# Performance work log

Measured on AMD Instinct MI355X. Metric: run time of the kernel, lower is better.

## Reference

```python
import jax, jax.numpy as jnp
import numpy as np

N_NODES = 50000
N_EDGES = 800000
IN_DIM = 128
HID = 64
HEADS = 4
OUT = 16
N_GRAPHS = 500
NEG_SLOPE = 0.2


def setup_inputs() -> dict:
    key = jax.random.key(0)
    ks = jax.random.split(key, 12)
    x = jax.random.normal(ks[0], (N_NODES, IN_DIM), dtype=jnp.float32)
    edge_index = jax.random.randint(ks[1], (2, N_EDGES), 0, N_NODES, dtype=jnp.int64)
    batch = jnp.sort(jax.random.randint(ks[2], (N_NODES,), 0, N_GRAPHS, dtype=jnp.int64))
    s1 = 1.0 / np.sqrt(IN_DIM)
    s2 = 1.0 / np.sqrt(HID)
    W1 = jax.random.normal(ks[3], (IN_DIM, HEADS * HID), dtype=jnp.float32) * s1
    a1_src = jax.random.normal(ks[4], (HEADS, HID), dtype=jnp.float32) * s2
    a1_dst = jax.random.normal(ks[5], (HEADS, HID), dtype=jnp.float32) * s2
    b1 = jnp.zeros((HID,), dtype=jnp.float32)
    W2 = jax.random.normal(ks[6], (HID, HEADS * HID), dtype=jnp.float32) * s2
    a2_src = jax.random.normal(ks[7], (HEADS, HID), dtype=jnp.float32) * s2
    a2_dst = jax.random.normal(ks[8], (HEADS, HID), dtype=jnp.float32) * s2
    b2 = jnp.zeros((HID,), dtype=jnp.float32)
    fcW = jax.random.normal(ks[9], (HID, OUT), dtype=jnp.float32) * s2
    fcb = jnp.zeros((OUT,), dtype=jnp.float32)
    return {"x": x, "edge_index": edge_index, "batch": batch,
            "W1": W1, "a1_src": a1_src, "a1_dst": a1_dst, "b1": b1,
            "W2": W2, "a2_src": a2_src, "a2_dst": a2_dst, "b2": b2,
            "fcW": fcW, "fcb": fcb}


def gat_conv(x, W, a_src, a_dst, b, src, dst):
    # PyG GATConv with concat=False: per-head linear, edge softmax over dst, head-mean.
    n = x.shape[0]
    h = (x @ W).reshape(n, HEADS, HID)          # [N,H,D]
    alpha_s = jnp.sum(h * a_src, axis=-1)        # [N,H]
    alpha_d = jnp.sum(h * a_dst, axis=-1)        # [N,H]
    e = jax.nn.leaky_relu(alpha_s[src] + alpha_d[dst], NEG_SLOPE)  # [E,H]
    emax = jax.ops.segment_max(e, dst, num_segments=n)
    ex = jnp.exp(e - emax[dst])
    denom = jax.ops.segment_sum(ex, dst, num_segments=n)
    alpha = ex / denom[dst]                      # [E,H], edge softmax per dst
    msg = h[src] * alpha[:, :, None]             # [E,H,D]
    out = jax.ops.segment_sum(msg, dst, num_segments=n)  # [N,H,D]
    return out.mean(axis=1) + b                  # concat=False -> head mean


def reference(x, edge_index, batch, W1, a1_src, a1_dst, b1, W2, a2_src, a2_dst, b2, fcW, fcb):
    n = x.shape[0]
    # PyG GATConv default add_self_loops=True
    loops = jnp.arange(n, dtype=edge_index.dtype)
    src = jnp.concatenate([edge_index[0], loops])
    dst = jnp.concatenate([edge_index[1], loops])
    h = jax.nn.relu(gat_conv(x, W1, a1_src, a1_dst, b1, src, dst))
    h = jax.nn.relu(gat_conv(h, W2, a2_src, a2_dst, b2, src, dst))
    # global_mean_pool over batch ids
    sums = jax.ops.segment_sum(h, batch, num_segments=N_GRAPHS)
    counts = jax.ops.segment_sum(jnp.ones((n,), dtype=h.dtype), batch, num_segments=N_GRAPHS)
    pooled = sums / jnp.clip(counts, 1.0)[:, None]
    return pooled @ fcW + fcb
```

## Files before the change

### kernel.cpp

```cpp
#include <hip/hip_runtime.h>
#include <hip/hip_bf16.h>
#include <hip/hip_fp16.h>

#define NN 50000
#define EE 800000
#define ETOT 850000
#define NG 500
#define NBLK ((NN + 255) / 256)

typedef __attribute__((ext_vector_type(8))) short bf16x8;
typedef __attribute__((ext_vector_type(4))) float f32x4;

__device__ __forceinline__ unsigned short bf16_rne(float v) {
    unsigned u = __float_as_uint(v);
    unsigned r = u + 0x7FFFu + ((u >> 16) & 1u);
    return (unsigned short)(r >> 16);
}

__device__ __forceinline__ int detect_stride(const int* __restrict__ ei,
                                             int tid, int* sflag) {
    if (tid < 64) {
        unsigned long long b = __ballot(ei[2 * tid + 1] != 0);
        if (tid == 0) *sflag = b ? 1 : 2;
    }
    __syncthreads();
    return *sflag;
}

__global__ __launch_bounds__(256) void k_prep(const int* __restrict__ ei,
                                              int* __restrict__ src32,
                                              int* __restrict__ dst32,
                                              int* __restrict__ deg) {
    __shared__ int sflag;
    int tid = threadIdx.x;
    int st = detect_stride(ei, tid, &sflag);
    int e = blockIdx.x * 256 + tid;
    if (e >= ETOT) return;
    int s, d;
    if (e < EE) {
        s = ei[(size_t)st * e];
        d = ei[(size_t)st * (EE + e)];
    } else {
        s = d = e - EE;
    }
    src32[e] = s;
    dst32[e] = d;
    atomicAdd(&deg[d], 1);
}

__global__ __launch_bounds__(256) void k_blocksum(const int* __restrict__ deg,
                                                  int* __restrict__ bsum) {
    __shared__ int l[256];
    int gid = blockIdx.x * 256 + threadIdx.x;
    int tid = threadIdx.x;
    l[tid] = (gid < NN) ? deg[gid] : 0;
    __syncthreads();
    for (int o = 128; o > 0; o >>= 1) {
        if (tid < o) l[tid] += l[tid + o];
        __syncthreads();
    }
    if (tid == 0) bsum[blockIdx.x] = l[0];
}

__global__ __launch_bounds__(256) void k_scan_bsum(const int* __restrict__ bsum,
                                                   int* __restrict__ boff) {
    __shared__ int l[256];
    int tid = threadIdx.x;
    int v = (tid < NBLK) ? bsum[tid] : 0;
    l[tid] = v;
    __syncthreads();
    for (int d = 1; d < 256; d <<= 1) {
        int t = (tid >= d) ? l[tid - d] : 0;
        __syncthreads();
        l[tid] += t;
        __syncthreads();
    }
    if (tid < NBLK) boff[tid] = l[tid] - v;
}

__global__ __launch_bounds__(256) void k_scan_final(const int* __restrict__ deg,
                                                    const int* __restrict__ boff,
                                                    int* __restrict__ rowptr,
                                                    int* __restrict__ cursor) {
    __shared__ int l[256];
    int gid = blockIdx.x * 256 + threadIdx.x;
    int tid = threadIdx.x;
    int v = (gid < NN) ? deg[gid] : 0;
    l[tid] = v;
    __syncthreads();
    for (int d = 1; d < 256; d <<= 1) {
        int t = (tid >= d) ? l[tid - d] : 0;
        __syncthreads();
        l[tid] += t;
        __syncthreads();
    }
    int ex = l[tid] - v + boff[blockIdx.x];
    if (gid < NN) { rowptr[gid] = ex; cursor[gid] = ex; }
    if (gid == 0) rowptr[NN] = ETOT;
}

__global__ __launch_bounds__(256) void k_scatter(const int* __restrict__ src32,
                                                 const int* __restrict__ dst32,
                                                 int* __restrict__ cursor,
                                                 int* __restrict__ csr_src) {
    int e = blockIdx.x * 256 + threadIdx.x;
    if (e >= ETOT) return;
    int pos = atomicAdd(&cursor[dst32[e]], 1);
    csr_src[pos] = src32[e];
}

__device__ __forceinline__ void prepw_one(const float* __restrict__ W,
                                          const float* __restrict__ asrc,
                                          const float* __restrict__ adst,
                                          unsigned short* __restrict__ bhi,
                                          unsigned short* __restrict__ blo,
                                          float* __restrict__ ap,
                                          float* __restrict__ adp,
                                          int K, int t) {
    int j = t / K, k = t - j * K;
    int d = j >> 2, h = j & 3;
    float v = W[k * 256 + h * 64 + d];
    unsigned short hb = bf16_rne(v);
    float hf = __uint_as_float((unsigned)hb << 16);
    bhi[t] = hb;
    blo[t] = bf16_rne(v - hf);
    if (k == 0) { ap[j] = asrc[h * 64 + d]; adp[j] = adst[h * 64 + d]; }
}

__global__ __launch_bounds__(256) void k_prepw(
        const float* __restrict__ W1, const float* __restrict__ a1s,
        const float* __restrict__ a1d, const float* __restrict__ W2,
        const float* __restrict__ a2s, const float* __restrict__ a2d,
        unsigned short* __restrict__ b1h, unsigned short* __restrict__ b1l,
        unsigned short* __restrict__ b2h, unsigned short* __restrict__ b2l,
        float* __restrict__ ap1, float* __restrict__ adp1,
        float* __restrict__ ap2, float* __restrict__ adp2) {
    int g = blockIdx.x;
    if (g < 128) {
        prepw_one(W1, a1s, a1d, b1h, b1l, ap1, adp1, 128, g * 256 + threadIdx.x);
    } else {
        prepw_one(W2, a2s, a2d, b2h, b2l, ap2, adp2, 64, (g - 128) * 256 + threadIdx.x);
    }
}

template <int K>
__global__ __launch_bounds__(64) void k_gemm_mfma(
        const float* __restrict__ A,
        const unsigned short* __restrict__ Bhi,
        const unsigned short* __restrict__ Blo,
        const float* __restrict__ aperm,
        const float* __restrict__ adperm,
        __half* __restrict__ C16,
        float* __restrict__ os,
        float* __restrict__ od, int M) {
    const int NC = K / 32;
    int lane = threadIdx.x;
    int l = lane & 15, q = lane >> 4;
    int m0 = blockIdx.x * 32;

    bf16x8 ahi[2][NC], alo[2][NC];
#pragma unroll
    for (int t = 0; t < 2; ++t) {
        int row = m0 + t * 16 + l;
        if (row >= M) row = M - 1;
        const float* arow = A + (size_t)row * K + q * 8;
#pragma unroll
        for (int c = 0; c < NC; ++c) {
            float4 v0 = *(const float4*)(arow + c * 32);
            float4 v1 = *(const float4*)(arow + c * 32 + 4);
            float vv[8] = {v0.x, v0.y, v0.z, v0.w, v1.x, v1.y, v1.z, v1.w};
#pragma unroll
            for (int j = 0; j < 8; ++j) {
                unsigned short hb = bf16_rne(vv[j]);
                float hf = __uint_as_float((unsigned)hb << 16);
                ahi[t][c][j] = (short)hb;
                alo[t][c][j] = (short)bf16_rne(vv[j] - hf);
            }
        }
    }

    float ps[2][4] = {}, pd[2][4] = {};
    const size_t brow = (size_t)l * K + q * 8;
#pragma unroll 2
    for (int n = 0; n < 16; ++n) {
        const unsigned short* bh = Bhi + (size_t)(n * 16) * K + brow;
        const unsigned short* bl = Blo + (size_t)(n * 16) * K + brow;
        bf16x8 bhf[NC], blf[NC];
#pragma unroll
        for (int c = 0; c < NC; ++c) {
            bhf[c] = *(const bf16x8*)(bh + c * 32);
            blf[c] = *(const bf16x8*)(bl + c * 32);
        }
        f32x4 acc0 = {0.f, 0.f, 0.f, 0.f}, acc1 = {0.f, 0.f, 0.f, 0.f};
#pragma unroll
        for (int c = 0; c < NC; ++c) {
            acc0 = __builtin_amdgcn_mfma_f32_16x16x32_bf16(ahi[0][c], bhf[c], acc0, 0, 0, 0);
            acc1 = __builtin_amdgcn_mfma_f32_16x16x32_bf16(ahi[1][c], bhf[c], acc1, 0, 0, 0);
            acc0 = __builtin_amdgcn_mfma_f32_16x16x32_bf16(ahi[0][c], blf[c], acc0, 0, 0, 0);
            acc1 = __builtin_amdgcn_mfma_f32_16x16x32_bf16(ahi[1][c], blf[c], acc1, 0, 0, 0);
            acc0 = __builtin_amdgcn_mfma_f32_16x16x32_bf16(alo[0][c], bhf[c], acc0, 0, 0, 0);
            acc1 = __builtin_amdgcn_mfma_f32_16x16x32_bf16(alo[1][c], bhf[c], acc1, 0, 0, 0);
        }
        float av = aperm[n * 16 + l], dv = adperm[n * 16 + l];
#pragma unroll
        for (int r = 0; r < 4; ++r) {
            ps[0][r] += acc0[r] * av; pd[0][r] += acc0[r] * dv;
            ps[1][r] += acc1[r] * av; pd[1][r] += acc1[r] * dv;
            int gm0 = m0 + q * 4 + r;
            if (gm0 < M) C16[(size_t)gm0 * 256 + n * 16 + l] = __float2half(acc0[r]);
            int gm1 = m0 + 16 + q * 4 + r;
            if (gm1 < M) C16[(size_t)gm1 * 256 + n * 16 + l] = __float2half(acc1[r]);
        }
    }
#pragma unroll
    for (int t = 0; t < 2; ++t)
#pragma unroll
        for (int r = 0; r < 4; ++r) {
            ps[t][r] += __shfl_xor(ps[t][r], 4);
            ps[t][r] += __shfl_xor(ps[t][r], 8);
            pd[t][r] += __shfl_xor(pd[t][r], 4);
            pd[t][r] += __shfl_xor(pd[t][r], 8);
        }
    if (l < 4) {
#pragma unroll
        for (int t = 0; t < 2; ++t)
#pragma unroll
            for (int r = 0; r < 4; ++r) {
                int gm = m0 + t * 16 + q * 4 + r;
                if (gm < M) {
                    os[(size_t)gm * 4 + l] = ps[t][r];
                    od[(size_t)gm * 4 + l] = pd[t][r];
                }
            }
    }
}

__device__ __forceinline__ float lrelu_exp(float x) {
    x = x > 0.f ? x : 0.2f * x;
    return __expf(x);
}

__global__ __launch_bounds__(256) void k_aggr(const int* __restrict__ rowptr,
                                              const int* __restrict__ csr_src,
                                              const float* __restrict__ as_,
                                              const float* __restrict__ ad_,
                                              const __half* __restrict__ h16,
                                              const float* __restrict__ bias,
                                              float* __restrict__ out) {
    __shared__ float als[4][256];
    __shared__ int sss[4][64];
    int w = threadIdx.x >> 6;
    int lane = threadIdx.x & 63;
    int d = blockIdx.x * 4 + w;
    if (d >= NN) return;
    int beg = rowptr[d], end = rowptr[d + 1];
    float4 adv = *(const float4*)(ad_ + d * 4);

    int s0 = 0;
    float4 u0 = make_float4(0.f, 0.f, 0.f, 0.f);
    float4 den = make_float4(0.f, 0.f, 0.f, 0.f);
    int i0 = beg + lane;
    if (i0 < end) {
        s0 = csr_src[i0];
        float4 sv = *(const float4*)(as_ + s0 * 4);
        u0.x = lrelu_exp(sv.x + adv.x);
        u0.y = lrelu_exp(sv.y + adv.y);
        u0.z = lrelu_exp(sv.z + adv.z);
        u0.w = lrelu_exp(sv.w + adv.w);
        den = u0;
    }
    for (int i = i0 + 64; i < end; i += 64) {
        int s = csr_src[i];
        float4 sv = *(const float4*)(as_ + s * 4);
        den.x += lrelu_exp(sv.x + adv.x);
        den.y += lrelu_exp(sv.y + adv.y);
        den.z += lrelu_exp(sv.z + adv.z);
        den.w += lrelu_exp(sv.w + adv.w);
    }
#pragma unroll
    for (int off = 32; off > 0; off >>= 1) {
        den.x += __shfl_xor(den.x, off);
        den.y += __shfl_xor(den.y, off);
        den.z += __shfl_xor(den.z, off);
        den.w += __shfl_xor(den.w, off);
    }
    float4 dinv = make_float4(0.25f / den.x, 0.25f / den.y,
                              0.25f / den.z, 0.25f / den.w);
    float4 al0 = make_float4(u0.x * dinv.x, u0.y * dinv.y,
                             u0.z * dinv.z, u0.w * dinv.w);
    *(float4*)&als[w][lane * 4] = al0;
    sss[w][lane] = s0;

    int cnt = end - beg;
    if (cnt > 64) cnt = 64;
    int cnt4 = (cnt + 3) & ~3;
    float acc = 0.f;
    int4 sq = *(const int4*)&sss[w][0];
    uint2 r0 = *(const uint2*)(h16 + (size_t)sq.x * 256 + lane * 4);
    uint2 r1 = *(const uint2*)(h16 + (size_t)sq.y * 256 + lane * 4);
    uint2 r2 = *(const uint2*)(h16 + (size_t)sq.z * 256 + lane * 4);
    uint2 r3 = *(const uint2*)(h16 + (size_t)sq.w * 256 + lane * 4);
    for (int j = 0; j < cnt4; j += 4) {
        int jn = (j + 4) & 63;
        int4 sn = *(const int4*)&sss[w][jn];
        uint2 n0 = *(const uint2*)(h16 + (size_t)sn.x * 256 + lane * 4);
        uint2 n1 = *(const uint2*)(h16 + (size_t)sn.y * 256 + lane * 4);
        uint2 n2 = *(const uint2*)(h16 + (size_t)sn.z * 256 + lane * 4);
        uint2 n3 = *(const uint2*)(h16 + (size_t)sn.w * 256 + lane * 4);
        float4 a0 = *(const float4*)&als[w][j * 4];
        float4 a1 = *(const float4*)&als[w][j * 4 + 4];
        float4 a2 = *(const float4*)&als[w][j * 4 + 8];
        float4 a3 = *(const float4*)&als[w][j * 4 + 12];
        float2 fa, fb;
        fa = __half22float2(*(const __half2*)&r0.x);
        fb = __half22float2(*(const __half2*)&r0.y);
        acc += a0.x * fa.x + a0.y * fa.y + a0.z * fb.x + a0.w * fb.y;
        fa = __half22float2(*(const __half2*)&r1.x);
        fb = __half22float2(*(const __half2*)&r1.y);
        acc += a1.x * fa.x + a1.y * fa.y + a1.z * fb.x + a1.w * fb.y;
        fa = __half22float2(*(const __half2*)&r2.x);
        fb = __half22float2(*(const __half2*)&r2.y);
        acc += a2.x * fa.x + a2.y * fa.y + a2.z * fb.x + a2.w * fb.y;
        fa = __half22float2(*(const __half2*)&r3.x);
        fb = __half22float2(*(const __half2*)&r3.y);
        acc += a3.x * fa.x + a3.y * fa.y + a3.z * fb.x + a3.w * fb.y;
        r0 = n0; r1 = n1; r2 = n2; r3 = n3;
    }
    for (int chunk = beg + 64; chunk < end; chunk += 64) {
        int i = chunk + lane;
        int s = 0;
        float4 al = make_float4(0.f, 0.f, 0.f, 0.f);
        if (i < end) {
            s = csr_src[i];
            float4 sv = *(const float4*)(as_ + s * 4);
            al.x = lrelu_exp(sv.x + adv.x) * dinv.x;
            al.y = lrelu_exp(sv.y + adv.y) * dinv.y;
            al.z = lrelu_exp(sv.z + adv.z) * dinv.z;
            al.w = lrelu_exp(sv.w + adv.w) * dinv.w;
        }
        int cc = end - chunk;
        if (cc > 64) cc = 64;
        for (int j = 0; j < cc; ++j) {
            int sj = __shfl(s, j);
            float a0 = __shfl(al.x, j), a1 = __shfl(al.y, j);
            float a2 = __shfl(al.z, j), a3 = __shfl(al.w, j);
            uint2 raw = *(const uint2*)(h16 + (size_t)sj * 256 + lane * 4);
            float2 fa = __half22float2(*(const __half2*)&raw.x);
            float2 fb = __half22float2(*(const __half2*)&raw.y);
            acc += a0 * fa.x + a1 * fa.y + a2 * fb.x + a3 * fb.y;
        }
    }
    float v = acc + bias[lane];
    out[d * 64 + lane] = v > 0.f ? v : 0.f;
}

__global__ __launch_bounds__(256) void k_pool_fc(const float* __restrict__ x3,
                                                 const int* __restrict__ batch,
                                                 const int* __restrict__ ei,
                                                 const float* __restrict__ fcW,
                                                 const float* __restrict__ fcb,
                                                 float* __restrict__ out) {
    __shared__ int sflag;
    int tid = threadIdx.x, lane = tid & 63, w = tid >> 6;
    int st = detect_stride(ei, tid, &sflag);
    int g = blockIdx.x;
    int lo = 0, hi = NN;
    while (lo < hi) { int mid = (lo + hi) >> 1; if (batch[(size_t)st * mid] < g) lo = mid + 1; else hi = mid; }
    int start = lo;
    hi = NN;
    while (lo < hi) { int mid = (lo + hi) >> 1; if (batch[(size_t)st * mid] < g + 1) lo = mid + 1; else hi = mid; }
    int end = lo;
    float sum = 0.f;
    for (int n = start + w; n < end; n += 4) sum += x3[n * 64 + lane];
    __shared__ float ls[4][64];
    ls[w][lane] = sum;
    __syncthreads();
    if (w == 0) {
        float c = (float)(end - start);
        if (c < 1.f) c = 1.f;
        float p = (ls[0][lane] + ls[1][lane] + ls[2][lane] + ls[3][lane]) / c;
#pragma unroll
        for (int o = 0; o < 16; ++o) {
            float v = p * fcW[lane * 16 + o];
#pragma unroll
            for (int off = 32; off > 0; off >>= 1) v += __shfl_down(v, off);
            if (lane == 0) out[g * 16 + o] = v + fcb[o];
        }
    }
}

extern "C" void kernel_launch(void* const* d_in, const int* in_sizes, int n_in,
                              void* d_out, int out_size, void* d_ws, size_t ws_size,
                              hipStream_t stream) {
    const float* x   = (const float*)d_in[0];
    const int*   ei  = (const int*)d_in[1];
    const int*   bat = (const int*)d_in[2];
    const float* W1  = (const float*)d_in[3];
    const float* a1s = (const float*)d_in[4];
    const float* a1d = (const float*)d_in[5];
    const float* b1  = (const float*)d_in[6];
    const float* W2  = (const float*)d_in[7];
    const float* a2s = (const float*)d_in[8];
    const float* a2d = (const float*)d_in[9];
    const float* b2  = (const float*)d_in[10];
    const float* fcW = (const float*)d_in[11];
    const float* fcb = (const float*)d_in[12];
    float* out = (float*)d_out;

    float* ws = (float*)d_ws;
    __half* h16  = (__half*)(ws + 256);
    float* as_   = (float*)(h16 + (size_t)NN * 256);
    float* ad_   = as_ + NN * 4;
    float* xacc  = ad_ + NN * 4;
    int* src32   = (int*)(xacc + (size_t)NN * 64);
    int* dst32   = src32 + ETOT;
    int* deg     = dst32 + ETOT;
    int* rowptr  = deg + NN;
    int* cursor  = rowptr + NN + 1;
    int* csr_src = cursor + NN;
    int* bsum    = csr_src + ETOT;
    int* boff    = bsum + NBLK;
    char* p = (char*)(boff + NBLK);
    p = (char*)(((size_t)p + 255) & ~(size_t)255);
    unsigned short* bt1h = (unsigned short*)p; p += 256 * 128 * 2;
    unsigned short* bt1l = (unsigned short*)p; p += 256 * 128 * 2;
    unsigned short* bt2h = (unsigned short*)p; p += 256 * 64 * 2;
    unsigned short* bt2l = (unsigned short*)p; p += 256 * 64 * 2;
    float* ap1  = (float*)p; p += 256 * 4;
    float* adp1 = (float*)p; p += 256 * 4;
    float* ap2  = (float*)p; p += 256 * 4;
    float* adp2 = (float*)p; p += 256 * 4;

    const int eb = (ETOT + 255) / 256;
    const int wb = (NN * 64 + 255) / 256;

    hipMemsetAsync(deg, 0, NN * sizeof(int), stream);
    k_prep<<<eb, 256, 0, stream>>>(ei, src32, dst32, deg);
    k_prepw<<<192, 256, 0, stream>>>(W1, a1s, a1d, W2, a2s, a2d,
                                     bt1h, bt1l, bt2h, bt2l,
                                     ap1, adp1, ap2, adp2);
    k_blocksum<<<NBLK, 256, 0, stream>>>(deg, bsum);
    k_scan_bsum<<<1, 256, 0, stream>>>(bsum, boff);
    k_scan_final<<<NBLK, 256, 0, stream>>>(deg, boff, rowptr, cursor);
    k_scatter<<<eb, 256, 0, stream>>>(src32, dst32, cursor, csr_src);

    const int gg = (NN + 31) / 32;
    k_gemm_mfma<128><<<gg, 64, 0, stream>>>(x, bt1h, bt1l, ap1, adp1, h16, as_, ad_, NN);
    k_aggr<<<wb, 256, 0, stream>>>(rowptr, csr_src, as_, ad_, h16, b1, xacc);
    k_gemm_mfma<64><<<gg, 64, 0, stream>>>(xacc, bt2h, bt2l, ap2, adp2, h16, as_, ad_, NN);
    k_aggr<<<wb, 256, 0, stream>>>(rowptr, csr_src, as_, ad_, h16, b2, xacc);
    k_pool_fc<<<NG, 256, 0, stream>>>(xacc, bat, ei, fcW, fcb, out);
}
```

Before: 379.1 us.

## Fuse preprocessing launches and use fp16 dot2 for first-chunk aggregation

Merges the edge-prep and weight-prep kernels into one launch, and folds the single-block scan of block sums into each scan_final block, removing two kernel launches. In the aggregation kernel, the first chunk's attention weights are stored in shared memory as packed fp16 pairs and combined with the gathered fp16 features via the fdot2 intrinsic instead of converting to fp32 and doing scalar FMAs. This cuts shared-memory traffic and ALU work, but rounds the attention coefficients to fp16, which adds some precision error. Each scan_final block now redundantly rescans all the block sums.

Result: no change. 379.1 us (median of 2 runs) (+0.0%).

```diff
diff --git a/kernel.cpp b/kernel.cpp
--- a/kernel.cpp
+++ b/kernel.cpp
@@ -7,9 +7,17 @@
 #define ETOT 850000
 #define NG 500
 #define NBLK ((NN + 255) / 256)
+#define EB ((ETOT + 255) / 256)
 
 typedef __attribute__((ext_vector_type(8))) short bf16x8;
 typedef __attribute__((ext_vector_type(4))) float f32x4;
+typedef _Float16 h2f __attribute__((ext_vector_type(2)));
+
+__device__ __forceinline__ h2f as_h2(unsigned u) {
+    union { unsigned u; h2f h; } x;
+    x.u = u;
+    return x.h;
+}
 
 __device__ __forceinline__ unsigned short bf16_rne(float v) {
     unsigned u = __float_as_uint(v);
@@ -25,88 +33,6 @@
     }
     __syncthreads();
     return *sflag;
-}
-
-__global__ __launch_bounds__(256) void k_prep(const int* __restrict__ ei,
-                                              int* __restrict__ src32,
-                                              int* __restrict__ dst32,
-                                              int* __restrict__ deg) {
-    __shared__ int sflag;
-    int tid = threadIdx.x;
-    int st = detect_stride(ei, tid, &sflag);
-    int e = blockIdx.x * 256 + tid;
-    if (e >= ETOT) return;
-    int s, d;
-    if (e < EE) {
-        s = ei[(size_t)st * e];
-        d = ei[(size_t)st * (EE + e)];
-    } else {
-        s = d = e - EE;
-    }
-    src32[e] = s;
-    dst32[e] = d;
-    atomicAdd(&deg[d], 1);
-}
-
-__global__ __launch_bounds__(256) void k_blocksum(const int* __restrict__ deg,
-                                                  int* __restrict__ bsum) {
-    __shared__ int l[256];
-    int gid = blockIdx.x * 256 + threadIdx.x;
-    int tid = threadIdx.x;
-    l[tid] = (gid < NN) ? deg[gid] : 0;
-    __syncthreads();
-    for (int o = 128; o > 0; o >>= 1) {
-        if (tid < o) l[tid] += l[tid + o];
-        __syncthreads();
-    }
-    if (tid == 0) bsum[blockIdx.x] = l[0];
-}
-
-__global__ __launch_bounds__(256) void k_scan_bsum(const int* __restrict__ bsum,
-                                                   int* __restrict__ boff) {
-    __shared__ int l[256];
-    int tid = threadIdx.x;
-    int v = (tid < NBLK) ? bsum[tid] : 0;
-    l[tid] = v;
-    __syncthreads();
-    for (int d = 1; d < 256; d <<= 1) {
-        int t = (tid >= d) ? l[tid - d] : 0;
-        __syncthreads();
-        l[tid] += t;
-        __syncthreads();
-    }
-    if (tid < NBLK) boff[tid] = l[tid] - v;
-}
-
-__global__ __launch_bounds__(256) void k_scan_final(const int* __restrict__ deg,
-                                                    const int* __restrict__ boff,
-                                                    int* __restrict__ rowptr,
-                                                    int* __restrict__ cursor) {
-    __shared__ int l[256];
-    int gid = blockIdx.x * 256 + threadIdx.x;
-    int tid = threadIdx.x;
-    int v = (gid < NN) ? deg[gid] : 0;
-    l[tid] = v;
-    __syncthreads();
-    for (int d = 1; d < 256; d <<= 1) {
-        int t = (tid >= d) ? l[tid - d] : 0;
-        __syncthreads();
-        l[tid] += t;
-        __syncthreads();
-    }
-    int ex = l[tid] - v + boff[blockIdx.x];
-    if (gid < NN) { rowptr[gid] = ex; cursor[gid] = ex; }
-    if (gid == 0) rowptr[NN] = ETOT;
-}
-
-__global__ __launch_bounds__(256) void k_scatter(const int* __restrict__ src32,
-                                                 const int* __restrict__ dst32,
-                                                 int* __restrict__ cursor,
-                                                 int* __restrict__ csr_src) {
-    int e = blockIdx.x * 256 + threadIdx.x;
-    if (e >= ETOT) return;
-    int pos = atomicAdd(&cursor[dst32[e]], 1);
-    csr_src[pos] = src32[e];
 }
 
 __device__ __forceinline__ void prepw_one(const float* __restrict__ W,
@@ -127,7 +53,9 @@
     if (k == 0) { ap[j] = asrc[h * 64 + d]; adp[j] = adst[h * 64 + d]; }
 }
 
-__global__ __launch_bounds__(256) void k_prepw(
+__global__ __launch_bounds__(256) void k_prep(
+        const int* __restrict__ ei, int* __restrict__ src32,
+        int* __restrict__ dst32, int* __restrict__ deg,
         const float* __restrict__ W1, const float* __restrict__ a1s,
         const float* __restrict__ a1d, const float* __restrict__ W2,
         const float* __restrict__ a2s, const float* __restrict__ a2d,
@@ -135,12 +63,86 @@
         unsigned short* __restrict__ b2h, unsigned short* __restrict__ b2l,
         float* __restrict__ ap1, float* __restrict__ adp1,
         float* __restrict__ ap2, float* __restrict__ adp2) {
-    int g = blockIdx.x;
-    if (g < 128) {
-        prepw_one(W1, a1s, a1d, b1h, b1l, ap1, adp1, 128, g * 256 + threadIdx.x);
+    int blk = blockIdx.x;
+    if (blk >= EB) {
+        int g = blk - EB;
+        if (g < 128)
+            prepw_one(W1, a1s, a1d, b1h, b1l, ap1, adp1, 128, g * 256 + threadIdx.x);
+        else
+            prepw_one(W2, a2s, a2d, b2h, b2l, ap2, adp2, 64, (g - 128) * 256 + threadIdx.x);
+        return;
+    }
+    __shared__ int sflag;
+    int tid = threadIdx.x;
+    int st = detect_stride(ei, tid, &sflag);
+    int e = blk * 256 + tid;
+    if (e >= ETOT) return;
+    int s, d;
+    if (e < EE) {
+        s = ei[(size_t)st * e];
+        d = ei[(size_t)st * (EE + e)];
     } else {
-        prepw_one(W2, a2s, a2d, b2h, b2l, ap2, adp2, 64, (g - 128) * 256 + threadIdx.x);
-    }
+        s = d = e - EE;
+    }
+    src32[e] = s;
+    dst32[e] = d;
+    atomicAdd(&deg[d], 1);
+}
+
+__global__ __launch_bounds__(256) void k_blocksum(const int* __restrict__ deg,
+                                                  int* __restrict__ bsum) {
+    __shared__ int l[256];
+    int gid = blockIdx.x * 256 + threadIdx.x;
+    int tid = threadIdx.x;
+    l[tid] = (gid < NN) ? deg[gid] : 0;
+    __syncthreads();
+    for (int o = 128; o > 0; o >>= 1) {
+        if (tid < o) l[tid] += l[tid + o];
+        __syncthreads();
+    }
+    if (tid == 0) bsum[blockIdx.x] = l[0];
+}
+
+__global__ __launch_bounds__(256) void k_scan_final(const int* __restrict__ deg,
+                                                    const int* __restrict__ bsum,
+                                                    int* __restrict__ rowptr,
+                                                    int* __restrict__ cursor) {
+    __shared__ int lb[256];
+    __shared__ int l[256];
+    int tid = threadIdx.x;
+    int vb = (tid < NBLK) ? bsum[tid] : 0;
+    lb[tid] = vb;
+    __syncthreads();
+    for (int d = 1; d < 256; d <<= 1) {
+        int t = (tid >= d) ? lb[tid - d] : 0;
+        __syncthreads();
+        lb[tid] += t;
+        __syncthreads();
+    }
+    int boffb = lb[blockIdx.x] - bsum[blockIdx.x];
+    int gid = blockIdx.x * 256 + tid;
+    int v = (gid < NN) ? deg[gid] : 0;
+    l[tid] = v;
+    __syncthreads();
+    for (int d = 1; d < 256; d <<= 1) {
+        int t = (tid >= d) ? l[tid - d] : 0;
+        __syncthreads();
+        l[tid] += t;
+        __syncthreads();
+    }
+    int ex = l[tid] - v + boffb;
+    if (gid < NN) { rowptr[gid] = ex; cursor[gid] = ex; }
+    if (gid == 0) rowptr[NN] = ETOT;
+}
+
+__global__ __launch_bounds__(256) void k_scatter(const int* __restrict__ src32,
+                                                 const int* __restrict__ dst32,
+                                                 int* __restrict__ cursor,
+                                                 int* __restrict__ csr_src) {
+    int e = blockIdx.x * 256 + threadIdx.x;
+    if (e >= ETOT) return;
+    int pos = atomicAdd(&cursor[dst32[e]], 1);
+    csr_src[pos] = src32[e];
 }
 
 template <int K>
@@ -247,7 +249,7 @@
                                               const __half* __restrict__ h16,
                                               const float* __restrict__ bias,
                                               float* __restrict__ out) {
-    __shared__ float als[4][256];
+    __shared__ uint2 als16[4][64];
     __shared__ int sss[4][64];
     int w = threadIdx.x >> 6;
     int lane = threadIdx.x & 63;
@@ -286,10 +288,12 @@
     }
     float4 dinv = make_float4(0.25f / den.x, 0.25f / den.y,
                               0.25f / den.z, 0.25f / den.w);
-    float4 al0 = make_float4(u0.x * dinv.x, u0.y * dinv.y,
-                             u0.z * dinv.z, u0.w * dinv.w);
-    *(float4*)&als[w][lane * 4] = al0;
-    sss[w][lane] = s0;
+    {
+        __half2 q0 = __floats2half2_rn(u0.x * dinv.x, u0.y * dinv.y);
+        __half2 q1 = __floats2half2_rn(u0.z * dinv.z, u0.w * dinv.w);
+        als16[w][lane] = make_uint2(*(unsigned*)&q0, *(unsigned*)&q1);
+        sss[w][lane] = s0;
+    }
 
     int cnt = end - beg;
     if (cnt > 64) cnt = 64;
@@ -307,23 +311,16 @@
         uint2 n1 = *(const uint2*)(h16 + (size_t)sn.y * 256 + lane * 4);
         uint2 n2 = *(const uint2*)(h16 + (size_t)sn.z * 256 + lane * 4);
         uint2 n3 = *(const uint2*)(h16 + (size_t)sn.w * 256 + lane * 4);
-        float4 a0 = *(const float4*)&als[w][j * 4];
-        float4 a1 = *(const float4*)&als[w][j * 4 + 4];
-        float4 a2 = *(const float4*)&als[w][j * 4 + 8];
-        float4 a3 = *(const float4*)&als[w][j * 4 + 12];
-        float2 fa, fb;
-        fa = __half22float2(*(const __half2*)&r0.x);
-        fb = __half22float2(*(const __half2*)&r0.y);
-        acc += a0.x * fa.x + a0.y * fa.y + a0.z * fb.x + a0.w * fb.y;
-        fa = __half22float2(*(const __half2*)&r1.x);
-        fb = __half22float2(*(const __half2*)&r1.y);
-        acc += a1.x * fa.x + a1.y * fa.y + a1.z * fb.x + a1.w * fb.y;
-        fa = __half22float2(*(const __half2*)&r2.x);
-        fb = __half22float2(*(const __half2*)&r2.y);
-        acc += a2.x * fa.x + a2.y * fa.y + a2.z * fb.x + a2.w * fb.y;
-        fa = __half22float2(*(const __half2*)&r3.x);
-        fb = __half22float2(*(const __half2*)&r3.y);
-        acc += a3.x * fa.x + a3.y * fa.y + a3.z * fb.x + a3.w * fb.y;
+        uint4 A01 = *(const uint4*)&als16[w][j];
+        uint4 A23 = *(const uint4*)&als16[w][j + 2];
+        acc = __builtin_amdgcn_fdot2(as_h2(r0.x), as_h2(A01.x), acc, false);
+        acc = __builtin_amdgcn_fdot2(as_h2(r0.y), as_h2(A01.y), acc, false);
+        acc = __builtin_amdgcn_fdot2(as_h2(r1.x), as_h2(A01.z), acc, false);
+        acc = __builtin_amdgcn_fdot2(as_h2(r1.y), as_h2(A01.w), acc, false);
+        acc = __builtin_amdgcn_fdot2(as_h2(r2.x), as_h2(A23.x), acc, false);
+        acc = __builtin_amdgcn_fdot2(as_h2(r2.y), as_h2(A23.y), acc, false);
+        acc = __builtin_amdgcn_fdot2(as_h2(r3.x), as_h2(A23.z), acc, false);
+        acc = __builtin_amdgcn_fdot2(as_h2(r3.y), as_h2(A23.w), acc, false);
         r0 = n0; r1 = n1; r2 = n2; r3 = n3;
     }
     for (int chunk = beg + 64; chunk < end; chunk += 64) {
@@ -419,8 +416,7 @@
     int* cursor  = rowptr + NN + 1;
     int* csr_src = cursor + NN;
     int* bsum    = csr_src + ETOT;
-    int* boff    = bsum + NBLK;
-    char* p = (char*)(boff + NBLK);
+    char* p = (char*)(bsum + NBLK);
     p = (char*)(((size_t)p + 255) & ~(size_t)255);
     unsigned short* bt1h = (unsigned short*)p; p += 256 * 128 * 2;
     unsigned short* bt1l = (unsigned short*)p; p += 256 * 128 * 2;
@@ -431,18 +427,16 @@
     float* ap2  = (float*)p; p += 256 * 4;
     float* adp2 = (float*)p; p += 256 * 4;
 
-    const int eb = (ETOT + 255) / 256;
     const int wb = (NN * 64 + 255) / 256;
 
     hipMemsetAsync(deg, 0, NN * sizeof(int), stream);
-    k_prep<<<eb, 256, 0, stream>>>(ei, src32, dst32, deg);
-    k_prepw<<<192, 256, 0, stream>>>(W1, a1s, a1d, W2, a2s, a2d,
-                                     bt1h, bt1l, bt2h, bt2l,
-                                     ap1, adp1, ap2, adp2);
+    k_prep<<<EB + 192, 256, 0, stream>>>(ei, src32, dst32, deg,
+                                         W1, a1s, a1d, W2, a2s, a2d,
+                                         bt1h, bt1l, bt2h, bt2l,
+                                         ap1, adp1, ap2, adp2);
     k_blocksum<<<NBLK, 256, 0, stream>>>(deg, bsum);
-    k_scan_bsum<<<1, 256, 0, stream>>>(bsum, boff);
-    k_scan_final<<<NBLK, 256, 0, stream>>>(deg, boff, rowptr, cursor);
-    k_scatter<<<eb, 256, 0, stream>>>(src32, dst32, cursor, csr_src);
+    k_scan_final<<<NBLK, 256, 0, stream>>>(deg, bsum, rowptr, cursor);
+    k_scatter<<<EB, 256, 0, stream>>>(src32, dst32, cursor, csr_src);
 
     const int gg = (NN + 31) / 32;
     k_gemm_mfma<128><<<gg, 64, 0, stream>>>(x, bt1h, bt1l, ap1, adp1, h16, as_, ad_, NN);
```
